# Kernel tuning notes

Measured on AMD Instinct MI355X. Metric: run time of the kernel, lower is better.

Reference implementation:

```python
import jax, jax.numpy as jnp
import numpy as np

CHUNK = 1024
HEAD_DIM = 128

def setup_inputs() -> dict:
    key = jax.random.key(0)
    k1, k2, k3 = jax.random.split(key, 3)
    B, H, S, D = 2, 16, 4096, HEAD_DIM
    q = jax.random.normal(k1, (B, H, S, D), dtype=jnp.float32)
    k = jax.random.normal(k2, (B, H, S, D), dtype=jnp.float32)
    v = jax.random.normal(k3, (B, H, S, D), dtype=jnp.float32)
    return {"q": q, "k": k, "v": v}

def reference(q, k, v):
    # Faithful to the torch module INCLUDING its masking bug: for every chunk
    # the triu mask uses diagonal=1 in chunk-local coordinates, so chunk-local
    # query row i attends only keys j<=i, i.e. only the first CHUNK keys matter.
    B, H, S, D = q.shape
    scale = D ** (-0.5)
    n = S // CHUNK
    qc = q.reshape(B, H, n, CHUNK, D)           # [B,H,n,C,D]
    kc = k[:, :, :CHUNK, :]                      # [B,H,C,D]
    vc = v[:, :, :CHUNK, :]                      # [B,H,C,D]
    scores = jnp.einsum('bhnid,bhjd->bhnij', qc, kc) * scale  # [B,H,n,C,C]
    mask = jnp.triu(jnp.ones((CHUNK, CHUNK), dtype=bool), 1)   # j > i masked
    scores = jnp.where(mask, -jnp.inf, scores)
    probs = jax.nn.softmax(scores, axis=-1)
    out = jnp.einsum('bhnij,bhjd->bhnid', probs, vc)
    return out.reshape(B, H, S, D)
```

## Files before the change

### kernel.cpp

```cpp
#include <hip/hip_runtime.h>


typedef __attribute__((ext_vector_type(8))) short bfrag_t;
typedef __attribute__((ext_vector_type(4))) float f32x4;
typedef unsigned short u16;
typedef unsigned int   u32;

#define SEQ     4096
#define SCHUNK  1024
#define HD      128
#define QBLK    64
#define KBLK    64
#define NTILE   16
#define TILE_E  8192

__device__ __forceinline__ u16 f2bf(float f) {
    union { float f; unsigned u; } x; x.f = f;
    unsigned r = x.u + 0x7fffu + ((x.u >> 16) & 1u);
    return (u16)(r >> 16);
}

__global__ __launch_bounds__(256)
void mea_prep(const float* __restrict__ kg, const float* __restrict__ vg,
              u16* __restrict__ wsK, u16* __restrict__ wsV)
{
    const int tid  = threadIdx.x;
    const int tile = blockIdx.x;
    const int bh = tile >> 4, kt = tile & 15;
    const long gsrc = (long)bh * SEQ * HD + (long)kt * KBLK * HD;
    const long gdst = (long)tile * TILE_E;

#pragma unroll
    for (int i = 0; i < 4; ++i) {
        int oid = i * 256 + tid;
        int j = oid >> 4, s = oid & 15;
        const float* kp = kg + gsrc + j * HD + s * 8;
        float4 a = *(const float4*)kp;
        float4 b = *(const float4*)(kp + 4);
        bfrag_t f;
        f[0]=f2bf(a.x); f[1]=f2bf(a.y); f[2]=f2bf(a.z); f[3]=f2bf(a.w);
        f[4]=f2bf(b.x); f[5]=f2bf(b.y); f[6]=f2bf(b.z); f[7]=f2bf(b.w);
        *(bfrag_t*)(wsK + gdst + j * 128 + ((s ^ (j & 15)) * 8)) = f;
    }
#pragma unroll
    for (int i = 0; i < 4; ++i) {
        int oid = i * 256 + tid;
        int jo = oid >> 7, d = oid & 127;
        const float* vp = vg + gsrc + jo * 8 * HD + d;
        bfrag_t f;
#pragma unroll
        for (int jj = 0; jj < 8; ++jj) f[jj] = f2bf(vp[jj * HD]);
        int d2 = d >> 1;
        int S  = (jo + ((d & 1) << 3)) ^ (d2 & 15);
        *(bfrag_t*)(wsV + gdst + d2 * 128 + S * 8) = f;
    }
}

__global__ __launch_bounds__(256, 2)
void mea_main(const float* __restrict__ qg, const u16* __restrict__ wsK,
              const u16* __restrict__ wsV, float* __restrict__ og)
{
    __shared__ __align__(16) u16 K_s[2][TILE_E];
    __shared__ __align__(16) u16 V_s[2][TILE_E];
    __shared__ __align__(16) u16 P_s[4][16 * 72];

    const int tid  = threadIdx.x;
    const int lane = tid & 63;
    const int wv   = tid >> 6;
    const int l15  = lane & 15;
    const int grp  = lane >> 4;

    const int x   = blockIdx.x & 7;
    const int idx = blockIdx.x >> 3;
    const int qt  = 15 - (idx >> 4);
    const int sub = idx & 15;
    const int bh  = x * 4 + (sub >> 2);
    const int ch  = sub & 3;

    const long qbase = ((long)bh * SEQ + ch * SCHUNK + qt * QBLK) * HD;
    const u16* Kb = wsK + (long)bh * NTILE * TILE_E;
    const u16* Vb = wsV + (long)bh * NTILE * TILE_E;

    bfrag_t qf[4];
    {
        const float qs = 0.12751723f;
        const float* qp = qg + qbase + (wv * 16 + l15) * HD + grp * 8;
#pragma unroll
        for (int ks = 0; ks < 4; ++ks) {
            float4 a = *(const float4*)(qp + ks * 32);
            float4 b = *(const float4*)(qp + ks * 32 + 4);
            bfrag_t f;
            f[0] = f2bf(a.x * qs); f[1] = f2bf(a.y * qs);
            f[2] = f2bf(a.z * qs); f[3] = f2bf(a.w * qs);
            f[4] = f2bf(b.x * qs); f[5] = f2bf(b.y * qs);
            f[6] = f2bf(b.z * qs); f[7] = f2bf(b.w * qs);
            qf[ks] = f;
        }
    }

    float m = -1e30f, lsum = 0.f;
    f32x4 oacc[8];
#pragma unroll
    for (int i = 0; i < 8; ++i) oacc[i] = (f32x4){0.f, 0.f, 0.f, 0.f};

    const int ntiles = qt + 1;

    bfrag_t kpre[4], vpre[4];
    const int soff = wv * 2048 + lane * 8;

    {
        const u16* ks = Kb + soff;
        const u16* vs = Vb + soff;
#pragma unroll
        for (int c = 0; c < 4; ++c) {
            kpre[c] = *(const bfrag_t*)(ks + c * 512);
            vpre[c] = *(const bfrag_t*)(vs + c * 512);
        }
#pragma unroll
        for (int c = 0; c < 4; ++c) {
            *(bfrag_t*)(&K_s[0][soff + c * 512]) = kpre[c];
            *(bfrag_t*)(&V_s[0][soff + c * 512]) = vpre[c];
        }
    }

    int cur = 0;
    for (int kt = 0; kt < ntiles; ++kt) {
        const bool pre = (kt + 1 < ntiles);
        if (pre) {
            const u16* ks = Kb + (long)(kt + 1) * TILE_E + soff;
            const u16* vs = Vb + (long)(kt + 1) * TILE_E + soff;
#pragma unroll
            for (int c = 0; c < 4; ++c) {
                kpre[c] = *(const bfrag_t*)(ks + c * 512);
                vpre[c] = *(const bfrag_t*)(vs + c * 512);
            }
        }
        asm volatile("s_waitcnt lgkmcnt(0)" ::: "memory");
        __builtin_amdgcn_s_barrier();

        f32x4 sacc[4];
#pragma unroll
        for (int jb = 0; jb < 4; ++jb) {
            f32x4 acc = (f32x4){0.f, 0.f, 0.f, 0.f};
            int j = jb * 16 + l15;
#pragma unroll
            for (int ks = 0; ks < 4; ++ks) {
                int slot = (ks * 4 + grp) ^ (j & 15);
                bfrag_t kf = *(const bfrag_t*)(&K_s[cur][j * 128 + slot * 8]);
                acc = __builtin_amdgcn_mfma_f32_16x16x32_bf16(kf, qf[ks], acc, 0, 0, 0);
            }
            sacc[jb] = acc;
        }

        float sv[16];
        float smax = -1e30f;
        if (kt == qt) {
            const int lq = wv * 16 + l15;
#pragma unroll
            for (int jb = 0; jb < 4; ++jb)
#pragma unroll
                for (int r = 0; r < 4; ++r) {
                    int lj = jb * 16 + grp * 4 + r;
                    float s = (lj <= (qt * 0 + (wv * 16 + l15))) ? sacc[jb][r] : -1e30f;
                    (void)lq;
                    sv[jb * 4 + r] = s;
                    smax = fmaxf(smax, s);
                }
        } else {
#pragma unroll
            for (int jb = 0; jb < 4; ++jb)
#pragma unroll
                for (int r = 0; r < 4; ++r) {
                    float s = sacc[jb][r];
                    sv[jb * 4 + r] = s;
                    smax = fmaxf(smax, s);
                }
        }
        smax = fmaxf(smax, __shfl_xor(smax, 16, 64));
        smax = fmaxf(smax, __shfl_xor(smax, 32, 64));

        if (!__all(smax - m <= 8.0f)) {
            float mnew = fmaxf(m, smax);
            float fac  = exp2f(m - mnew);
            lsum *= fac;
            float f0 = __shfl(fac, grp * 4 + 0, 64);
            float f1 = __shfl(fac, grp * 4 + 1, 64);
            float f2 = __shfl(fac, grp * 4 + 2, 64);
            float f3 = __shfl(fac, grp * 4 + 3, 64);
#pragma unroll
            for (int nb = 0; nb < 8; ++nb) {
                oacc[nb][0] *= f0; oacc[nb][1] *= f1;
                oacc[nb][2] *= f2; oacc[nb][3] *= f3;
            }
            m = mnew;
        }

        float psum = 0.f;
#pragma unroll
        for (int jb = 0; jb < 4; ++jb) {
            float p0 = exp2f(sv[jb*4+0] - m);
            float p1 = exp2f(sv[jb*4+1] - m);
            float p2 = exp2f(sv[jb*4+2] - m);
            float p3 = exp2f(sv[jb*4+3] - m);
            psum += (p0 + p1) + (p2 + p3);
            u32 w0, w1;
            asm("v_cvt_pk_bf16_f32 %0, %1, %2" : "=v"(w0) : "v"(p0), "v"(p1));
            asm("v_cvt_pk_bf16_f32 %0, %1, %2" : "=v"(w1) : "v"(p2), "v"(p3));
            uint2 w = {w0, w1};
            *(uint2*)(&P_s[wv][l15 * 72 + jb * 16 + grp * 4]) = w;
        }
        psum += __shfl_xor(psum, 16, 64);
        psum += __shfl_xor(psum, 32, 64);
        lsum += psum;

#pragma unroll
        for (int ks2 = 0; ks2 < 2; ++ks2) {
            bfrag_t pf = *(const bfrag_t*)(&P_s[wv][l15 * 72 + ks2 * 32 + grp * 8]);
#pragma unroll
            for (int nb = 0; nb < 8; ++nb) {
                int d  = nb * 16 + l15;
                int d2 = d >> 1;
                int S  = ((ks2 * 4 + grp) + ((d & 1) << 3)) ^ (d2 & 15);
                bfrag_t vf = *(const bfrag_t*)(&V_s[cur][d2 * 128 + S * 8]);
                oacc[nb] = __builtin_amdgcn_mfma_f32_16x16x32_bf16(pf, vf, oacc[nb], 0, 0, 0);
            }
        }

        if (pre) {
            int b = cur ^ 1;
#pragma unroll
            for (int c = 0; c < 4; ++c) {
                *(bfrag_t*)(&K_s[b][soff + c * 512]) = kpre[c];
                *(bfrag_t*)(&V_s[b][soff + c * 512]) = vpre[c];
            }
        }
        cur ^= 1;
    }

    float inv = 1.f / lsum;
    float i0 = __shfl(inv, grp * 4 + 0, 64);
    float i1 = __shfl(inv, grp * 4 + 1, 64);
    float i2 = __shfl(inv, grp * 4 + 2, 64);
    float i3 = __shfl(inv, grp * 4 + 3, 64);
    float invs[4] = {i0, i1, i2, i3};
#pragma unroll
    for (int r = 0; r < 4; ++r) {
        float* op = og + qbase + (wv * 16 + grp * 4 + r) * HD + l15;
#pragma unroll
        for (int nb = 0; nb < 8; ++nb) op[nb * 16] = oacc[nb][r] * invs[r];
    }
}

extern "C" void kernel_launch(void* const* d_in, const int* in_sizes, int n_in,
                              void* d_out, int out_size, void* d_ws, size_t ws_size,
                              hipStream_t stream)
{
    (void)in_sizes; (void)n_in; (void)out_size; (void)ws_size;
    const float* q = (const float*)d_in[0];
    const float* k = (const float*)d_in[1];
    const float* v = (const float*)d_in[2];
    float* o = (float*)d_out;
    u16* wsK = (u16*)d_ws;
    u16* wsV = wsK + (size_t)32 * NTILE * TILE_E;
    mea_prep<<<dim3(512),  dim3(256), 0, stream>>>(k, v, wsK, wsV);
    mea_main<<<dim3(2048), dim3(256), 0, stream>>>(q, wsK, wsV, o);
}
```

Before: 84.74 us.

## Use 32x32 MFMA with register-resident P and direct global-to-LDS K/V loads

Rewrites the attention main loop around 32x32x16 bf16 MFMA. Each wave now handles 32 query rows from a different sequence chunk, so all four waves in a block share the same K/V tiles and the grid halves. The probability matrix stays in registers and is reshuffled with v_permlane32_swap instead of going through an LDS P buffer. K/V tiles are fetched with global_load_lds instead of staging through registers, MFMA sections are wrapped in s_setprio, and the output is written as float4 stores. This aims to cut LDS traffic, register staging and instruction overhead, at the cost of larger accumulators and more register pressure.

```diff
diff --git a/kernel.cpp b/kernel.cpp
--- a/kernel.cpp
+++ b/kernel.cpp
@@ -2,14 +2,13 @@
 
 
 typedef __attribute__((ext_vector_type(8))) short bfrag_t;
-typedef __attribute__((ext_vector_type(4))) float f32x4;
+typedef __attribute__((ext_vector_type(16))) float f32x16;
 typedef unsigned short u16;
 typedef unsigned int   u32;
 
 #define SEQ     4096
 #define SCHUNK  1024
 #define HD      128
-#define QBLK    64
 #define KBLK    64
 #define NTILE   16
 #define TILE_E  8192
@@ -56,198 +55,187 @@
     }
 }
 
+__device__ __forceinline__ void gll16(const u16* g, u16* l) {
+    __builtin_amdgcn_global_load_lds((const __attribute__((address_space(1))) u32*)g,
+                                     (__attribute__((address_space(3))) u32*)l, 16, 0, 0);
+}
+
 __global__ __launch_bounds__(256, 2)
 void mea_main(const float* __restrict__ qg, const u16* __restrict__ wsK,
               const u16* __restrict__ wsV, float* __restrict__ og)
 {
     __shared__ __align__(16) u16 K_s[2][TILE_E];
     __shared__ __align__(16) u16 V_s[2][TILE_E];
-    __shared__ __align__(16) u16 P_s[4][16 * 72];
 
     const int tid  = threadIdx.x;
     const int lane = tid & 63;
     const int wv   = tid >> 6;
-    const int l15  = lane & 15;
-    const int grp  = lane >> 4;
+    const int c31  = lane & 31;
+    const int hi   = lane >> 5;
 
     const int x   = blockIdx.x & 7;
     const int idx = blockIdx.x >> 3;
-    const int qt  = 15 - (idx >> 4);
-    const int sub = idx & 15;
-    const int bh  = x * 4 + (sub >> 2);
-    const int ch  = sub & 3;
-
-    const long qbase = ((long)bh * SEQ + ch * SCHUNK + qt * QBLK) * HD;
+    const int qt  = 31 - (idx >> 2);
+    const int bh  = x * 4 + (idx & 3);
+
+    const long rowbase = (long)bh * SEQ + (long)wv * SCHUNK + (long)qt * 32;
     const u16* Kb = wsK + (long)bh * NTILE * TILE_E;
     const u16* Vb = wsV + (long)bh * NTILE * TILE_E;
 
-    bfrag_t qf[4];
+    bfrag_t qf[8];
     {
         const float qs = 0.12751723f;
-        const float* qp = qg + qbase + (wv * 16 + l15) * HD + grp * 8;
-#pragma unroll
-        for (int ks = 0; ks < 4; ++ks) {
-            float4 a = *(const float4*)(qp + ks * 32);
-            float4 b = *(const float4*)(qp + ks * 32 + 4);
+        const float* qp = qg + (rowbase + c31) * HD + hi * 8;
+#pragma unroll
+        for (int ks = 0; ks < 8; ++ks) {
+            float4 a = *(const float4*)(qp + ks * 16);
+            float4 b = *(const float4*)(qp + ks * 16 + 4);
             bfrag_t f;
-            f[0] = f2bf(a.x * qs); f[1] = f2bf(a.y * qs);
-            f[2] = f2bf(a.z * qs); f[3] = f2bf(a.w * qs);
-            f[4] = f2bf(b.x * qs); f[5] = f2bf(b.y * qs);
-            f[6] = f2bf(b.z * qs); f[7] = f2bf(b.w * qs);
+            f[0]=f2bf(a.x*qs); f[1]=f2bf(a.y*qs); f[2]=f2bf(a.z*qs); f[3]=f2bf(a.w*qs);
+            f[4]=f2bf(b.x*qs); f[5]=f2bf(b.y*qs); f[6]=f2bf(b.z*qs); f[7]=f2bf(b.w*qs);
             qf[ks] = f;
         }
     }
 
+    f32x16 oacc[4];
+#pragma unroll
+    for (int d = 0; d < 4; ++d)
+#pragma unroll
+        for (int i = 0; i < 16; ++i) oacc[d][i] = 0.f;
+
     float m = -1e30f, lsum = 0.f;
-    f32x4 oacc[8];
-#pragma unroll
-    for (int i = 0; i < 8; ++i) oacc[i] = (f32x4){0.f, 0.f, 0.f, 0.f};
-
-    const int ntiles = qt + 1;
-
-    bfrag_t kpre[4], vpre[4];
-    const int soff = wv * 2048 + lane * 8;
-
-    {
-        const u16* ks = Kb + soff;
-        const u16* vs = Vb + soff;
-#pragma unroll
-        for (int c = 0; c < 4; ++c) {
-            kpre[c] = *(const bfrag_t*)(ks + c * 512);
-            vpre[c] = *(const bfrag_t*)(vs + c * 512);
-        }
-#pragma unroll
-        for (int c = 0; c < 4; ++c) {
-            *(bfrag_t*)(&K_s[0][soff + c * 512]) = kpre[c];
-            *(bfrag_t*)(&V_s[0][soff + c * 512]) = vpre[c];
-        }
+    const int nt = (qt >> 1) + 1;
+    const int gq = qt * 32 + c31;
+    const int so = wv * 2048 + lane * 8;
+
+#pragma unroll
+    for (int c = 0; c < 4; ++c) {
+        gll16(Kb + so + c * 512, &K_s[0][wv * 2048 + c * 512]);
+        gll16(Vb + so + c * 512, &V_s[0][wv * 2048 + c * 512]);
     }
 
     int cur = 0;
-    for (int kt = 0; kt < ntiles; ++kt) {
-        const bool pre = (kt + 1 < ntiles);
-        if (pre) {
-            const u16* ks = Kb + (long)(kt + 1) * TILE_E + soff;
-            const u16* vs = Vb + (long)(kt + 1) * TILE_E + soff;
+    for (int kt = 0; kt < nt; ++kt) {
+        __syncthreads();
+        if (kt + 1 < nt) {
+            const long t = (long)(kt + 1) * TILE_E;
 #pragma unroll
             for (int c = 0; c < 4; ++c) {
-                kpre[c] = *(const bfrag_t*)(ks + c * 512);
-                vpre[c] = *(const bfrag_t*)(vs + c * 512);
-            }
-        }
-        asm volatile("s_waitcnt lgkmcnt(0)" ::: "memory");
-        __builtin_amdgcn_s_barrier();
-
-        f32x4 sacc[4];
-#pragma unroll
-        for (int jb = 0; jb < 4; ++jb) {
-            f32x4 acc = (f32x4){0.f, 0.f, 0.f, 0.f};
-            int j = jb * 16 + l15;
-#pragma unroll
-            for (int ks = 0; ks < 4; ++ks) {
-                int slot = (ks * 4 + grp) ^ (j & 15);
-                bfrag_t kf = *(const bfrag_t*)(&K_s[cur][j * 128 + slot * 8]);
-                acc = __builtin_amdgcn_mfma_f32_16x16x32_bf16(kf, qf[ks], acc, 0, 0, 0);
-            }
-            sacc[jb] = acc;
-        }
-
-        float sv[16];
-        float smax = -1e30f;
-        if (kt == qt) {
-            const int lq = wv * 16 + l15;
-#pragma unroll
-            for (int jb = 0; jb < 4; ++jb)
-#pragma unroll
-                for (int r = 0; r < 4; ++r) {
-                    int lj = jb * 16 + grp * 4 + r;
-                    float s = (lj <= (qt * 0 + (wv * 16 + l15))) ? sacc[jb][r] : -1e30f;
-                    (void)lq;
-                    sv[jb * 4 + r] = s;
-                    smax = fmaxf(smax, s);
+                gll16(Kb + t + so + c * 512, &K_s[cur ^ 1][wv * 2048 + c * 512]);
+                gll16(Vb + t + so + c * 512, &V_s[cur ^ 1][wv * 2048 + c * 512]);
+            }
+        }
+
+        f32x16 sacc[2];
+#pragma unroll
+        for (int g = 0; g < 2; ++g)
+#pragma unroll
+            for (int i = 0; i < 16; ++i) sacc[g][i] = 0.f;
+
+        __builtin_amdgcn_s_setprio(1);
+#pragma unroll
+        for (int g = 0; g < 2; ++g) {
+            const int j = g * 32 + c31;
+            const u16* krow = &K_s[cur][j * 128];
+#pragma unroll
+            for (int ks = 0; ks < 8; ++ks) {
+                int slot = (ks * 2 + hi) ^ (c31 & 15);
+                bfrag_t kf = *(const bfrag_t*)(krow + slot * 8);
+                sacc[g] = __builtin_amdgcn_mfma_f32_32x32x16_bf16(kf, qf[ks], sacc[g], 0, 0, 0);
+            }
+        }
+        __builtin_amdgcn_s_setprio(0);
+
+        if (kt == nt - 1) {
+#pragma unroll
+            for (int g = 0; g < 2; ++g)
+#pragma unroll
+                for (int r = 0; r < 16; ++r) {
+                    int jl = kt * 64 + g * 32 + (r & 3) + 8 * (r >> 2) + 4 * hi;
+                    if (jl > gq) sacc[g][r] = -1e30f;
                 }
-        } else {
-#pragma unroll
-            for (int jb = 0; jb < 4; ++jb)
-#pragma unroll
-                for (int r = 0; r < 4; ++r) {
-                    float s = sacc[jb][r];
-                    sv[jb * 4 + r] = s;
-                    smax = fmaxf(smax, s);
-                }
-        }
-        smax = fmaxf(smax, __shfl_xor(smax, 16, 64));
-        smax = fmaxf(smax, __shfl_xor(smax, 32, 64));
-
-        if (!__all(smax - m <= 8.0f)) {
+        }
+
+        float smax = sacc[0][0];
+#pragma unroll
+        for (int g = 0; g < 2; ++g)
+#pragma unroll
+            for (int r = 0; r < 16; ++r) smax = fmaxf(smax, sacc[g][r]);
+        smax = fmaxf(smax, __shfl_xor(smax, 32));
+
+        if (__any(smax - m > 8.0f)) {
             float mnew = fmaxf(m, smax);
             float fac  = exp2f(m - mnew);
             lsum *= fac;
-            float f0 = __shfl(fac, grp * 4 + 0, 64);
-            float f1 = __shfl(fac, grp * 4 + 1, 64);
-            float f2 = __shfl(fac, grp * 4 + 2, 64);
-            float f3 = __shfl(fac, grp * 4 + 3, 64);
-#pragma unroll
-            for (int nb = 0; nb < 8; ++nb) {
-                oacc[nb][0] *= f0; oacc[nb][1] *= f1;
-                oacc[nb][2] *= f2; oacc[nb][3] *= f3;
-            }
+#pragma unroll
+            for (int d = 0; d < 4; ++d)
+#pragma unroll
+                for (int i = 0; i < 16; ++i) oacc[d][i] *= fac;
             m = mnew;
         }
 
         float psum = 0.f;
 #pragma unroll
-        for (int jb = 0; jb < 4; ++jb) {
-            float p0 = exp2f(sv[jb*4+0] - m);
-            float p1 = exp2f(sv[jb*4+1] - m);
-            float p2 = exp2f(sv[jb*4+2] - m);
-            float p3 = exp2f(sv[jb*4+3] - m);
-            psum += (p0 + p1) + (p2 + p3);
-            u32 w0, w1;
-            asm("v_cvt_pk_bf16_f32 %0, %1, %2" : "=v"(w0) : "v"(p0), "v"(p1));
-            asm("v_cvt_pk_bf16_f32 %0, %1, %2" : "=v"(w1) : "v"(p2), "v"(p3));
-            uint2 w = {w0, w1};
-            *(uint2*)(&P_s[wv][l15 * 72 + jb * 16 + grp * 4]) = w;
-        }
-        psum += __shfl_xor(psum, 16, 64);
-        psum += __shfl_xor(psum, 32, 64);
+        for (int g = 0; g < 2; ++g)
+#pragma unroll
+            for (int r = 0; r < 16; ++r) {
+                float p = exp2f(sacc[g][r] - m);
+                sacc[g][r] = p;
+                psum += p;
+            }
+        psum += __shfl_xor(psum, 32);
         lsum += psum;
 
-#pragma unroll
-        for (int ks2 = 0; ks2 < 2; ++ks2) {
-            bfrag_t pf = *(const bfrag_t*)(&P_s[wv][l15 * 72 + ks2 * 32 + grp * 8]);
-#pragma unroll
-            for (int nb = 0; nb < 8; ++nb) {
-                int d  = nb * 16 + l15;
-                int d2 = d >> 1;
-                int S  = ((ks2 * 4 + grp) + ((d & 1) << 3)) ^ (d2 & 15);
-                bfrag_t vf = *(const bfrag_t*)(&V_s[cur][d2 * 128 + S * 8]);
-                oacc[nb] = __builtin_amdgcn_mfma_f32_16x16x32_bf16(pf, vf, oacc[nb], 0, 0, 0);
-            }
-        }
-
-        if (pre) {
-            int b = cur ^ 1;
-#pragma unroll
-            for (int c = 0; c < 4; ++c) {
-                *(bfrag_t*)(&K_s[b][soff + c * 512]) = kpre[c];
-                *(bfrag_t*)(&V_s[b][soff + c * 512]) = vpre[c];
-            }
-        }
+        bfrag_t pfrag[4];
+#pragma unroll
+        for (int g = 0; g < 2; ++g) {
+            u32 W[8];
+#pragma unroll
+            for (int s = 0; s < 8; ++s)
+                asm("v_cvt_pk_bf16_f32 %0, %1, %2"
+                    : "=v"(W[s]) : "v"(sacc[g][2 * s]), "v"(sacc[g][2 * s + 1]));
+#pragma unroll
+            for (int u = 0; u < 2; ++u) {
+                u32 x0 = W[4 * u + 0], y0 = W[4 * u + 2];
+                u32 x1 = W[4 * u + 1], y1 = W[4 * u + 3];
+                asm volatile("v_permlane32_swap_b32 %0, %1" : "+v"(x0), "+v"(y0));
+                asm volatile("v_permlane32_swap_b32 %0, %1" : "+v"(x1), "+v"(y1));
+                union { u32 w[4]; bfrag_t f; } uu;
+                uu.w[0] = x0; uu.w[1] = x1; uu.w[2] = y0; uu.w[3] = y1;
+                pfrag[g * 2 + u] = uu.f;
+            }
+        }
+
+        __builtin_amdgcn_s_setprio(1);
+#pragma unroll
+        for (int dg = 0; dg < 4; ++dg) {
+            const int d  = dg * 32 + c31;
+            const int d2 = d >> 1;
+            const u16* vrow = &V_s[cur][d2 * 128];
+#pragma unroll
+            for (int jsl = 0; jsl < 4; ++jsl) {
+                int S = ((jsl * 2 + hi) + ((d & 1) << 3)) ^ (d2 & 15);
+                bfrag_t vf = *(const bfrag_t*)(vrow + S * 8);
+                oacc[dg] = __builtin_amdgcn_mfma_f32_32x32x16_bf16(vf, pfrag[jsl], oacc[dg], 0, 0, 0);
+            }
+        }
+        __builtin_amdgcn_s_setprio(0);
+
         cur ^= 1;
     }
 
     float inv = 1.f / lsum;
-    float i0 = __shfl(inv, grp * 4 + 0, 64);
-    float i1 = __shfl(inv, grp * 4 + 1, 64);
-    float i2 = __shfl(inv, grp * 4 + 2, 64);
-    float i3 = __shfl(inv, grp * 4 + 3, 64);
-    float invs[4] = {i0, i1, i2, i3};
-#pragma unroll
-    for (int r = 0; r < 4; ++r) {
-        float* op = og + qbase + (wv * 16 + grp * 4 + r) * HD + l15;
-#pragma unroll
-        for (int nb = 0; nb < 8; ++nb) op[nb * 16] = oacc[nb][r] * invs[r];
+#pragma unroll
+    for (int dg = 0; dg < 4; ++dg) {
+#pragma unroll
+        for (int rq = 0; rq < 4; ++rq) {
+            float4 v;
+            v.x = oacc[dg][rq * 4 + 0] * inv;
+            v.y = oacc[dg][rq * 4 + 1] * inv;
+            v.z = oacc[dg][rq * 4 + 2] * inv;
+            v.w = oacc[dg][rq * 4 + 3] * inv;
+            *(float4*)(og + (rowbase + c31) * HD + dg * 32 + rq * 8 + hi * 4) = v;
+        }
     }
 }
 
@@ -263,5 +251,5 @@
     u16* wsK = (u16*)d_ws;
     u16* wsV = wsK + (size_t)32 * NTILE * TILE_E;
     mea_prep<<<dim3(512),  dim3(256), 0, stream>>>(k, v, wsK, wsV);
-    mea_main<<<dim3(2048), dim3(256), 0, stream>>>(q, wsK, wsV, o);
-}
+    mea_main<<<dim3(1024), dim3(256), 0, stream>>>(q, wsK, wsV, o);
+}
```

New measurement: 83.38 us. Within noise of the previous version (-1.6%).
